# Performance work log

Hardware: AMD Instinct MI355X
Metric: run time of the kernel (lower is better)

The kernel has to match this reference:

```python
import jax, jax.numpy as jnp
import numpy as np

N = 100000
NEG_SLOPE = 0.2
EPS = 1e-16


def _gatconv(h_in, src, dst, W, a_src, a_dst, b):
    # h_in: [N, Fin]; src/dst: [E_tot] (self-loops included); W: [Fin, Fout]
    h = h_in @ W                                  # [N, Fout]
    alpha_s = h @ a_src                           # [N]
    alpha_d = h @ a_dst                           # [N]
    e = alpha_s[src] + alpha_d[dst]               # [E_tot]
    e = jnp.where(e > 0, e, NEG_SLOPE * e)        # leaky_relu
    m = jax.ops.segment_max(e, dst, num_segments=N)
    e = jnp.exp(e - m[dst])
    s = jax.ops.segment_sum(e, dst, num_segments=N)
    alpha = e / (s[dst] + EPS)                    # segment softmax over in-edges of each dst
    out = jax.ops.segment_sum(alpha[:, None] * h[src], dst, num_segments=N)
    return out + b


def setup_inputs() -> dict:
    key = jax.random.key(0)
    ks = jax.random.split(key, 10)
    Fin, Fh, Fo = 64, 64, 40
    E = 1600000
    x = jax.random.normal(ks[0], (N, Fin), dtype=jnp.float32)
    edge_index = jax.random.randint(ks[1], (2, E), 0, N, dtype=jnp.int64)
    g = 1.0 / np.sqrt(Fin)
    W1 = jax.random.uniform(ks[2], (Fin, Fh), jnp.float32, -g, g)
    a_src1 = jax.random.uniform(ks[3], (Fh,), jnp.float32, -g, g)
    a_dst1 = jax.random.uniform(ks[4], (Fh,), jnp.float32, -g, g)
    b1 = jnp.zeros((Fh,), jnp.float32)
    g2 = 1.0 / np.sqrt(Fh)
    W2 = jax.random.uniform(ks[5], (Fh, Fo), jnp.float32, -g2, g2)
    a_src2 = jax.random.uniform(ks[6], (Fo,), jnp.float32, -g2, g2)
    a_dst2 = jax.random.uniform(ks[7], (Fo,), jnp.float32, -g2, g2)
    b2 = jnp.zeros((Fo,), jnp.float32)
    return {"x": x, "edge_index": edge_index, "W1": W1, "a_src1": a_src1,
            "a_dst1": a_dst1, "b1": b1, "W2": W2, "a_src2": a_src2,
            "a_dst2": a_dst2, "b2": b2}


def reference(x, edge_index, W1, a_src1, a_dst1, b1, W2, a_src2, a_dst2, b2):
    # add self loops (PyG GATConv default)
    loops = jnp.arange(N, dtype=edge_index.dtype)
    src = jnp.concatenate([edge_index[0], loops])
    dst = jnp.concatenate([edge_index[1], loops])
    h = _gatconv(x, src, dst, W1, a_src1, a_dst1, b1)
    h = jax.nn.relu(h)  # dropout p=0 / eval -> no-op
    h = _gatconv(h, src, dst, W2, a_src2, a_dst2, b2)
    return jax.nn.log_softmax(h, axis=-1)
```

## Files before the change

### kernel.cpp

```cpp
#include <hip/hip_runtime.h>
#include <math.h>

#ifndef NEG_SLOPE
#define NEG_SLOPE 0.2f
#endif

#define BUCK_BITS 9
#define BUCK_SIZE 512
#define BUCK_CAP  12288
#define PA_ILP    8
#define SMAX      0x1FFFF

typedef __attribute__((ext_vector_type(8))) short bhalf8;
typedef __attribute__((ext_vector_type(4))) float f32x4;

__device__ __forceinline__ void get_edge(const void* ei, int is64, int e, int E,
                                         int& s, int& d) {
    if (e >= E) { s = e - E; d = s; return; }
    if (is64) {
        const long long* p = (const long long*)ei;
        s = (int)p[e];
        d = (int)p[(long long)E + e];
    } else {
        const int* p = (const int*)ei;
        s = p[e];
        d = p[E + e];
    }
}

__device__ __forceinline__ unsigned f2bf1(float x) {
    unsigned u = __float_as_uint(x);
    return (u + 0x7fffu + ((u >> 16) & 1u)) >> 16;
}

__global__ __launch_bounds__(256) void bin_gemm1(
    const void* __restrict__ ei, int E, int Etot, int binB, int gemmB, int period,
    int* __restrict__ fill, unsigned* __restrict__ pairs,
    const float* __restrict__ x, const float* __restrict__ W1,
    const float* __restrict__ avs, const float* __restrict__ avd,
    unsigned short* __restrict__ Hb, float* __restrict__ asn,
    float* __restrict__ adn, int N) {
    __shared__ __align__(16) char smem[4096];
    const int t = threadIdx.x;
    const int bi = blockIdx.x;
    const bool isBin = (bi % period) == 0;

    if (isBin) {
        const int bb = bi / period;
        int* cnt   = (int*)smem;
        int* goff  = cnt + 256;
        int* sflag = goff + 256;
        if (t < 64) {
            const int* p = (const int*)ei;
            int bad = 0;
            for (int j = 0; j < 4; ++j) bad |= (p[2 * (t * 4 + j) + 1] != 0);
            unsigned long long m = __ballot(bad);
            if (t == 0) *sflag = (m == 0ull) ? 1 : 0;
        }
        cnt[t] = 0;
        __syncthreads();
        const int is64 = *sflag;
        const int base = bb * (256 * PA_ILP) + t;
        int s[PA_ILP], d[PA_ILP], r[PA_ILP];
        bool ok[PA_ILP];
#pragma unroll
        for (int u = 0; u < PA_ILP; ++u) {
            int e = base + u * 256;
            ok[u] = (e < Etot);
            s[u] = d[u] = 0;
            if (ok[u]) get_edge(ei, is64, e, E, s[u], d[u]);
        }
#pragma unroll
        for (int u = 0; u < PA_ILP; ++u)
            if (ok[u]) r[u] = atomicAdd(&cnt[d[u] >> BUCK_BITS], 1);
        __syncthreads();
        if (cnt[t] > 0) goff[t] = atomicAdd(&fill[t], cnt[t]);
        __syncthreads();
#pragma unroll
        for (int u = 0; u < PA_ILP; ++u) {
            if (ok[u]) {
                int b = d[u] >> BUCK_BITS;
                int idx = goff[b] + r[u];
                if (idx < BUCK_CAP)
                    pairs[(size_t)b * BUCK_CAP + idx] =
                        (unsigned)s[u] | ((unsigned)(d[u] & (BUCK_SIZE - 1)) << 17);
            }
        }
    } else {
        const int gi = bi - bi / period - 1;
        if (gi >= gemmB) return;
        const int lane = t & 63;
        const int w    = t >> 6;
        const int rloc = lane & 15;
        const int kg   = lane >> 4;
        const int base = gi * 64;
        const int row  = base + w * 16 + rloc;
        const int rowc = (row < N) ? row : (N - 1);

        bhalf8 xh[2], xl[2];
        {
            const float* xr = x + (size_t)rowc * 64;
#pragma unroll
            for (int ks = 0; ks < 2; ++ks) {
                const int k0 = kg * 8 + ks * 32;
                float4 a0 = *(const float4*)(xr + k0);
                float4 a1 = *(const float4*)(xr + k0 + 4);
                float av[8] = {a0.x, a0.y, a0.z, a0.w, a1.x, a1.y, a1.z, a1.w};
                bhalf8 h8, l8;
#pragma unroll
                for (int j = 0; j < 8; ++j) {
                    unsigned hb_ = f2bf1(av[j]);
                    float hf = __uint_as_float(hb_ << 16);
                    h8[j] = (short)hb_;
                    l8[j] = (short)f2bf1(av[j] - hf);
                }
                xh[ks] = h8;
                xl[ks] = l8;
            }
        }

        f32x4 dacc[4];
#pragma unroll
        for (int ct = 0; ct < 4; ++ct) dacc[ct] = (f32x4){0.f, 0.f, 0.f, 0.f};

#pragma unroll
        for (int ct = 0; ct < 4; ++ct) {
            const int col = ct * 16 + rloc;
#pragma unroll
            for (int ks = 0; ks < 2; ++ks) {
                const int k0 = kg * 8 + ks * 32;
                bhalf8 bh, bl;
#pragma unroll
                for (int j = 0; j < 8; ++j) {
                    float wv_ = W1[(size_t)(k0 + j) * 64 + col];
                    unsigned hb_ = f2bf1(wv_);
                    float hf = __uint_as_float(hb_ << 16);
                    bh[j] = (short)hb_;
                    bl[j] = (short)f2bf1(wv_ - hf);
                }
                dacc[ct] = __builtin_amdgcn_mfma_f32_16x16x32_bf16(xh[ks], bh, dacc[ct], 0, 0, 0);
                dacc[ct] = __builtin_amdgcn_mfma_f32_16x16x32_bf16(xl[ks], bh, dacc[ct], 0, 0, 0);
                dacc[ct] = __builtin_amdgcn_mfma_f32_16x16x32_bf16(xh[ks], bl, dacc[ct], 0, 0, 0);
            }
        }

        float sa[4], sd[4];
#pragma unroll
        for (int ct = 0; ct < 4; ++ct) {
            sa[ct] = avs[ct * 16 + rloc];
            sd[ct] = avd[ct * 16 + rloc];
        }
#pragma unroll
        for (int i = 0; i < 4; ++i) {
            float ps = 0.f, pd = 0.f;
#pragma unroll
            for (int ct = 0; ct < 4; ++ct) {
                float h = dacc[ct][i];
                ps += h * sa[ct];
                pd += h * sd[ct];
            }
#pragma unroll
            for (int off = 1; off < 16; off <<= 1) {
                ps += __shfl_xor(ps, off);
                pd += __shfl_xor(pd, off);
            }
            const int gr = base + w * 16 + kg * 4 + i;
            if (gr < N) {
                if (rloc == 0) { asn[gr] = ps; adn[gr] = pd; }
#pragma unroll
                for (int ct = 0; ct < 4; ++ct)
                    Hb[(size_t)gr * 64 + ct * 16 + rloc] =
                        (unsigned short)f2bf1(dacc[ct][i]);
            }
        }
    }
}

__global__ __launch_bounds__(256) void bucket_csr(
    const unsigned* __restrict__ pairs, const int* __restrict__ fill,
    int* __restrict__ row_ptr, int* __restrict__ csr_src, int N, int nbuck) {
    __shared__ int cnt[BUCK_SIZE];
    __shared__ int offs[BUCK_SIZE];
    __shared__ int sbase[256];
    __shared__ int stot;
    const int t = threadIdx.x;
    if (t < 64) {
        int v[4];
        int loc = 0;
#pragma unroll
        for (int i = 0; i < 4; ++i) {
            int idx = t * 4 + i;
            v[i] = (idx < nbuck) ? fill[idx] : 0;
            loc += v[i];
        }
        int x = loc;
        for (int off = 1; off < 64; off <<= 1) {
            int y = __shfl_up(x, off);
            if (t >= off) x += y;
        }
        int run = x - loc;
#pragma unroll
        for (int i = 0; i < 4; ++i) {
            int idx = t * 4 + i;
            if (idx < 256) sbase[idx] = run;
            run += v[i];
        }
        if (t == 63) stot = x;
    }
    cnt[t] = 0; cnt[t + 256] = 0;
    __syncthreads();

    const int b = blockIdx.x;
    const int gb = sbase[b];
    int m = fill[b];
    if (m > BUCK_CAP) m = BUCK_CAP;
    if (b == 0 && t == 0) row_ptr[N] = stot;
    const unsigned* bp = pairs + (size_t)b * BUCK_CAP;

    int i = t;
    for (; i + 768 < m; i += 1024) {
        unsigned p0 = bp[i], p1 = bp[i + 256], p2 = bp[i + 512], p3 = bp[i + 768];
        atomicAdd(&cnt[p0 >> 17], 1);
        atomicAdd(&cnt[p1 >> 17], 1);
        atomicAdd(&cnt[p2 >> 17], 1);
        atomicAdd(&cnt[p3 >> 17], 1);
    }
    for (; i < m; i += 256) atomicAdd(&cnt[bp[i] >> 17], 1);
    __syncthreads();

    if (t < 64) {
        int v[8];
        int loc = 0;
#pragma unroll
        for (int j = 0; j < 8; ++j) { v[j] = cnt[t * 8 + j]; loc += v[j]; }
        int x = loc;
        for (int off = 1; off < 64; off <<= 1) {
            int y = __shfl_up(x, off);
            if (t >= off) x += y;
        }
        int run = x - loc;
#pragma unroll
        for (int j = 0; j < 8; ++j) { offs[t * 8 + j] = gb + run; run += v[j]; }
    }
    __syncthreads();

    const int base_d = b << BUCK_BITS;
    for (int k = t; k < BUCK_SIZE; k += 256) {
        int d = base_d + k;
        if (d < N) row_ptr[d] = offs[k];
    }
    __syncthreads();

    i = t;
    for (; i + 768 < m; i += 1024) {
        unsigned p0 = bp[i], p1 = bp[i + 256], p2 = bp[i + 512], p3 = bp[i + 768];
        csr_src[atomicAdd(&offs[p0 >> 17], 1)] = p0 & SMAX;
        csr_src[atomicAdd(&offs[p1 >> 17], 1)] = p1 & SMAX;
        csr_src[atomicAdd(&offs[p2 >> 17], 1)] = p2 & SMAX;
        csr_src[atomicAdd(&offs[p3 >> 17], 1)] = p3 & SMAX;
    }
    for (; i < m; i += 256) {
        unsigned p = bp[i];
        csr_src[atomicAdd(&offs[p >> 17], 1)] = p & SMAX;
    }
}

__device__ __forceinline__ void bf16x8_fma(uint4 hv, float w, float* acc) {
    const unsigned* u = (const unsigned*)&hv;
#pragma unroll
    for (int i = 0; i < 4; ++i) {
        float lo = __uint_as_float(u[i] << 16);
        float hi = __uint_as_float(u[i] & 0xffff0000u);
        acc[2 * i]     += w * lo;
        acc[2 * i + 1] += w * hi;
    }
}

__global__ __launch_bounds__(256) void agg1_gemm2(
    const int* __restrict__ row_ptr, const int* __restrict__ csr_src,
    const float* __restrict__ asn1, const float* __restrict__ adn1,
    const unsigned short* __restrict__ Hb, const float* __restrict__ b1,
    const float* __restrict__ W2, const float* __restrict__ a_s2,
    const float* __restrict__ a_d2, unsigned short* __restrict__ Hb2,
    float* __restrict__ asn2, float* __restrict__ adn2, int N) {
    __shared__ __align__(16) unsigned short rb16[16][72];
    __shared__ float sa2[48], sd2[48], sb1[64];
    __shared__ float sps3[3][16], spd3[3][16];
    const int t = threadIdx.x;
    if (t < 48) {
        sa2[t] = (t < 40) ? a_s2[t] : 0.f;
        sd2[t] = (t < 40) ? a_d2[t] : 0.f;
    }
    if (t >= 64 && t < 128) sb1[t - 64] = b1[t - 64];

    const int lane = t & 63;
    const int wv   = t >> 6;
    const int tile = (wv < 3) ? wv : 0;

    bhalf8 bfr[2];
    {
        const int col = tile * 16 + (lane & 15);
        const int kb  = (lane >> 4) * 8;
        const bool cv = col < 40;
#pragma unroll
        for (int ks = 0; ks < 2; ++ks) {
            bhalf8 bb;
#pragma unroll
            for (int j = 0; j < 8; ++j) {
                float v = cv ? W2[(size_t)(kb + 32 * ks + j) * 40 + col] : 0.f;
                bb[j] = (short)f2bf1(v);
            }
            bfr[ks] = bb;
        }
    }
    __syncthreads();

    const int sub     = lane & 15;
    const int half    = sub >> 3;
    const int q       = sub & 7;
    const int grpbase = lane & 48;
    const int slot    = t >> 4;
    const int node    = blockIdx.x * 16 + slot;
    const bool valid  = node < N;
    const int nd      = valid ? node : N - 1;

    const int r0 = row_ptr[nd], r1 = row_ptr[nd + 1];
    const int deg = r1 - r0;
    const float add = adn1[nd];

    float acc[8];
#pragma unroll
    for (int i = 0; i < 8; ++i) acc[i] = 0.f;

    int   sA = 0, sB = 0;
    float wA = 0.f, wB = 0.f;
    {
        const bool vA = sub < deg;
        const bool vB = 16 + sub < deg;
        if (vA) sA = csr_src[r0 + sub];
        if (vB) sB = csr_src[r0 + 16 + sub];
        float aA = vA ? asn1[sA] : 0.f;
        float aB = vB ? asn1[sB] : 0.f;
        if (vA) { float v = aA + add; v = v > 0.f ? v : NEG_SLOPE * v; wA = __expf(v); }
        if (vB) { float v = aB + add; v = v > 0.f ? v : NEG_SLOPE * v; wB = __expf(v); }
    }
    float Ssum = wA + wB;

    {
        const int cnt = deg < 16 ? deg : 16;
        int se[8]; float we[8]; uint4 hv[8];
#pragma unroll
        for (int k = 0; k < 8; ++k) {
            int e = 2 * k + half;
            int sl = grpbase | (e & 15);
            se[k] = __shfl(sA, sl);
            float wk = __shfl(wA, sl);
            we[k] = (e < cnt) ? wk : 0.f;
        }
#pragma unroll
        for (int k = 0; k < 4; ++k)
            hv[k] = *(const uint4*)(Hb + (((unsigned)se[k] << 6) | (unsigned)(q << 3)));
        if (cnt > 8) {
#pragma unroll
            for (int k = 4; k < 8; ++k)
                hv[k] = *(const uint4*)(Hb + (((unsigned)se[k] << 6) | (unsigned)(q << 3)));
        }
#pragma unroll
        for (int k = 0; k < 4; ++k) bf16x8_fma(hv[k], we[k], acc);
        if (cnt > 8) {
#pragma unroll
            for (int k = 4; k < 8; ++k) bf16x8_fma(hv[k], we[k], acc);
        }
    }
    if (deg > 16) {
        const int cnt = (deg - 16) < 16 ? (deg - 16) : 16;
// ... 39 lines not shown
            for (int k = 0; k < 4; ++k) {
                int e = j + 2 * k + half;
                int src_lane = grpbase | (e & 15);
                se[k] = __shfl(s, src_lane);
                float wk = __shfl(w, src_lane);
                we[k] = (e < cnt) ? wk : 0.f;
            }
#pragma unroll
            for (int k = 0; k < 4; ++k)
                hv[k] = *(const uint4*)(Hb + (((unsigned)se[k] << 6) | (unsigned)(q << 3)));
#pragma unroll
            for (int k = 0; k < 4; ++k) bf16x8_fma(hv[k], we[k], acc);
        }
    }
#pragma unroll
    for (int i = 0; i < 8; ++i) acc[i] += __shfl_xor(acc[i], 8);
#pragma unroll
    for (int off = 1; off < 16; off <<= 1) Ssum += __shfl_xor(Ssum, off);
    const float inv = 1.f / (Ssum + 1e-16f);

    if (half == 0) {
        unsigned pk[4];
#pragma unroll
        for (int i = 0; i < 4; ++i) {
            float v0 = fmaxf(acc[2 * i]     * inv + sb1[q * 8 + 2 * i],     0.f);
            float v1 = fmaxf(acc[2 * i + 1] * inv + sb1[q * 8 + 2 * i + 1], 0.f);
            pk[i] = f2bf1(v0) | (f2bf1(v1) << 16);
        }
        *(uint4*)&rb16[slot][q * 8] = make_uint4(pk[0], pk[1], pk[2], pk[3]);
    }
    __syncthreads();

    if (wv < 3) {
        f32x4 dacc = {0.f, 0.f, 0.f, 0.f};
#pragma unroll
        for (int ks = 0; ks < 2; ++ks) {
            bhalf8 afr = *(const bhalf8*)&rb16[lane & 15][(lane >> 4) * 8 + 32 * ks];
            dacc = __builtin_amdgcn_mfma_f32_16x16x32_bf16(afr, bfr[ks], dacc, 0, 0, 0);
        }
        const int f   = tile * 16 + (lane & 15);
        const float saf = sa2[f];
        const float sdf = sd2[f];
        float psl = 0.f, pdl = 0.f;
#pragma unroll
        for (int i = 0; i < 4; ++i) {
            psl = dacc[i] * saf;
            pdl = dacc[i] * sdf;
#pragma unroll
            for (int off = 1; off < 16; off <<= 1) {
                psl += __shfl_xor(psl, off);
                pdl += __shfl_xor(pdl, off);
            }
            const int m  = (lane >> 4) * 4 + i;
            if ((lane & 15) == 0) { sps3[tile][m] = psl; spd3[tile][m] = pdl; }
            const int nn = blockIdx.x * 16 + m;
            if (f < 40 && nn < N)
                Hb2[(size_t)nn * 40 + f] = (unsigned short)f2bf1(dacc[i]);
        }
    }
    __syncthreads();
    if (t < 16) {
        const int nn = blockIdx.x * 16 + t;
        if (nn < N) {
            asn2[nn] = sps3[0][t] + sps3[1][t] + sps3[2][t];
            adn2[nn] = spd3[0][t] + spd3[1][t] + spd3[2][t];
        }
    }
}

__global__ __launch_bounds__(256) void agg2_lsm(
    const int* __restrict__ row_ptr, const int* __restrict__ csr_src,
    const float* __restrict__ asn, const float* __restrict__ adn,
    const unsigned short* __restrict__ Hb, const float* __restrict__ bias,
    float* __restrict__ out, int N) {
    const int lane    = threadIdx.x & 63;
    const int sub     = lane & 15;
    const int esl     = sub / 5;
    const int q5      = sub - esl * 5;
    const bool act    = sub < 15;
    const int qc      = act ? q5 : 0;
    const float qmask = act ? 1.f : 0.f;
    const int grpbase = lane & 48;
    const int node    = blockIdx.x * 16 + (threadIdx.x >> 4);
    const bool valid  = node < N;
    const int nd      = valid ? node : N - 1;

    const int r0 = row_ptr[nd], r1 = row_ptr[nd + 1];
    const int deg = r1 - r0;
    const float add = adn[nd];

    float acc[8];
#pragma unroll
    for (int i = 0; i < 8; ++i) acc[i] = 0.f;

    int   sA = 0, sB = 0;
    float wA = 0.f, wB = 0.f;
    {
        const bool vA = sub < deg;
        const bool vB = 16 + sub < deg;
        if (vA) sA = csr_src[r0 + sub];
        if (vB) sB = csr_src[r0 + 16 + sub];
        float aA = vA ? asn[sA] : 0.f;
        float aB = vB ? asn[sB] : 0.f;
        if (vA) { float v = aA + add; v = v > 0.f ? v : NEG_SLOPE * v; wA = __expf(v); }
        if (vB) { float v = aB + add; v = v > 0.f ? v : NEG_SLOPE * v; wB = __expf(v); }
    }
    float Ssum = wA + wB;

    {
        const int cnt = deg < 16 ? deg : 16;
        int se[6]; float we[6]; uint4 hv[6];
#pragma unroll
        for (int kk = 0; kk < 6; ++kk) {
            int e  = 3 * kk + esl;
            int el = (e < 16) ? e : 15;
            se[kk] = __shfl(sA, grpbase | el);
            float wk = __shfl(wA, grpbase | el) * qmask;
            we[kk] = (e < cnt) ? wk : 0.f;
        }
#pragma unroll
        for (int kk = 0; kk < 4; ++kk)
            hv[kk] = *(const uint4*)(Hb + ((unsigned)se[kk] * 40u + (unsigned)(qc << 3)));
        if (cnt > 12) {
#pragma unroll
            for (int kk = 4; kk < 6; ++kk)
                hv[kk] = *(const uint4*)(Hb + ((unsigned)se[kk] * 40u + (unsigned)(qc << 3)));
        }
#pragma unroll
        for (int kk = 0; kk < 4; ++kk) bf16x8_fma(hv[kk], we[kk], acc);
        if (cnt > 12) {
#pragma unroll
            for (int kk = 4; kk < 6; ++kk) bf16x8_fma(hv[kk], we[kk], acc);
        }
    }
    if (deg > 16) {
        const int cnt = (deg - 16) < 16 ? (deg - 16) : 16;
// ... 34 lines not shown
        }
        Ssum += w;
        for (int j = 0; j < cnt; j += 12) {
            int se[4]; float we[4]; uint4 hv[4];
#pragma unroll
            for (int k = 0; k < 4; ++k) {
                int e  = j + 3 * k + esl;
                int el = (e < 16) ? e : 15;
                se[k] = __shfl(s, grpbase | el);
                float wk = __shfl(w, grpbase | el) * qmask;
                we[k] = (e < cnt) ? wk : 0.f;
            }
#pragma unroll
            for (int k = 0; k < 4; ++k)
                hv[k] = *(const uint4*)(Hb + ((unsigned)se[k] * 40u + (unsigned)(qc << 3)));
#pragma unroll
            for (int k = 0; k < 4; ++k) bf16x8_fma(hv[k], we[k], acc);
        }
    }
#pragma unroll
    for (int i = 0; i < 8; ++i) {
        float a1 = __shfl(acc[i], grpbase + q5 + 5);
        float a2 = __shfl(acc[i], grpbase + q5 + 10);
        acc[i] += a1 + a2;
    }
#pragma unroll
    for (int off = 1; off < 16; off <<= 1) Ssum += __shfl_xor(Ssum, off);
    const float inv = 1.f / (Ssum + 1e-16f);
    const bool owner = act && (esl == 0);

    float val[8];
#pragma unroll
    for (int i = 0; i < 8; ++i) val[i] = acc[i] * inv + bias[qc * 8 + i];
    float mx = -3.0e38f;
    if (owner) {
#pragma unroll
        for (int i = 0; i < 8; ++i) mx = fmaxf(mx, val[i]);
    }
#pragma unroll
    for (int off = 1; off <= 8; off <<= 1) mx = fmaxf(mx, __shfl_xor(mx, off));
    float sm = 0.f;
    if (owner) {
#pragma unroll
        for (int i = 0; i < 8; ++i) sm += __expf(val[i] - mx);
    }
#pragma unroll
    for (int off = 1; off <= 8; off <<= 1) sm += __shfl_xor(sm, off);
    float ls = logf(sm) + mx;
    if (valid && owner) {
        float* op = out + (size_t)node * 40 + q5 * 8;
        ((float4*)op)[0] = make_float4(val[0] - ls, val[1] - ls, val[2] - ls, val[3] - ls);
        ((float4*)op)[1] = make_float4(val[4] - ls, val[5] - ls, val[6] - ls, val[7] - ls);
    }
}

extern "C" void kernel_launch(void* const* d_in, const int* in_sizes, int n_in,
                              void* d_out, int out_size, void* d_ws, size_t ws_size,
                              hipStream_t stream) {
    const float* x   = (const float*)d_in[0];
    const void*  ei  = d_in[1];
    const float* W1  = (const float*)d_in[2];
    const float* as1 = (const float*)d_in[3];
    const float* ad1 = (const float*)d_in[4];
    const float* b1  = (const float*)d_in[5];
    const float* W2  = (const float*)d_in[6];
    const float* as2 = (const float*)d_in[7];
    const float* ad2 = (const float*)d_in[8];
    const float* b2  = (const float*)d_in[9];
    float* out = (float*)d_out;

    const int N     = in_sizes[0] / 64;
    const int E     = in_sizes[1] / 2;
    const int Etot  = E + N;
    const int nbuck = (N + BUCK_SIZE - 1) >> BUCK_BITS;

    float* ws = (float*)d_ws;
    unsigned short* hb  = (unsigned short*)ws;  ws += (size_t)N * 32;
    unsigned short* hb2 = (unsigned short*)ws;  ws += (size_t)N * 20;
    float* asn1 = ws;              ws += N;
    float* adn1 = ws;              ws += N;
    float* asn2 = ws;              ws += N;
    float* adn2 = ws;              ws += N;
    int* row_ptr = (int*)ws;       ws += N + 1;
    int* csr_src = (int*)ws;       ws += Etot;
    int* fill   = (int*)ws;        ws += 256;
    unsigned* pairs = (unsigned*)ws;  ws += (size_t)256 * BUCK_CAP;

    const int binB   = (Etot + 256 * PA_ILP - 1) / (256 * PA_ILP);
    const int gemmB  = (N + 63) / 64;
    const int period = gemmB / binB + 2;
    const int grid1  = binB * period;
    const int AGG_B  = (N + 15) / 16;

    hipMemsetAsync(fill, 0, 256 * sizeof(int), stream);
    bin_gemm1<<<grid1, 256, 0, stream>>>(
        ei, E, Etot, binB, gemmB, period, fill, pairs,
        x, W1, as1, ad1, hb, asn1, adn1, N);
    bucket_csr<<<nbuck, 256, 0, stream>>>(pairs, fill, row_ptr, csr_src, N, nbuck);
    agg1_gemm2<<<AGG_B, 256, 0, stream>>>(
        row_ptr, csr_src, asn1, adn1, hb, b1, W2, as2, ad2, hb2, asn2, adn2, N);
    agg2_lsm<<<AGG_B, 256, 0, stream>>>(
        row_ptr, csr_src, asn2, adn2, hb2, b2, out, N);
}
```

Baseline: 220.1 us.

## Fuse bucket-to-CSR pass with first GEMM instead of edge binning

Result: slower. 231.9 us (+5.4%).

```diff
diff --git a/kernel.cpp b/kernel.cpp
--- a/kernel.cpp
+++ b/kernel.cpp
@@ -33,58 +33,145 @@
     return (u + 0x7fffu + ((u >> 16) & 1u)) >> 16;
 }
 
-__global__ __launch_bounds__(256) void bin_gemm1(
-    const void* __restrict__ ei, int E, int Etot, int binB, int gemmB, int period,
-    int* __restrict__ fill, unsigned* __restrict__ pairs,
+__global__ __launch_bounds__(256) void bin_pass(
+    const void* __restrict__ ei, int E, int Etot,
+    int* __restrict__ fill, unsigned* __restrict__ pairs) {
+    __shared__ int cnt[256];
+    __shared__ int goff[256];
+    __shared__ int sflag;
+    const int t = threadIdx.x;
+    if (t < 64) {
+        const int* p = (const int*)ei;
+        int bad = 0;
+        for (int j = 0; j < 4; ++j) bad |= (p[2 * (t * 4 + j) + 1] != 0);
+        unsigned long long m = __ballot(bad);
+        if (t == 0) sflag = (m == 0ull) ? 1 : 0;
+    }
+    cnt[t] = 0;
+    __syncthreads();
+    const int is64 = sflag;
+    const int base = blockIdx.x * (256 * PA_ILP) + t;
+    int s[PA_ILP], d[PA_ILP], r[PA_ILP];
+    bool ok[PA_ILP];
+#pragma unroll
+    for (int u = 0; u < PA_ILP; ++u) {
+        int e = base + u * 256;
+        ok[u] = (e < Etot);
+        s[u] = d[u] = 0;
+        if (ok[u]) get_edge(ei, is64, e, E, s[u], d[u]);
+    }
+#pragma unroll
+    for (int u = 0; u < PA_ILP; ++u)
+        if (ok[u]) r[u] = atomicAdd(&cnt[d[u] >> BUCK_BITS], 1);
+    __syncthreads();
+    if (cnt[t] > 0) goff[t] = atomicAdd(&fill[t], cnt[t]);
+    __syncthreads();
+#pragma unroll
+    for (int u = 0; u < PA_ILP; ++u) {
+        if (ok[u]) {
+            int b = d[u] >> BUCK_BITS;
+            int idx = goff[b] + r[u];
+            if (idx < BUCK_CAP)
+                pairs[(size_t)b * BUCK_CAP + idx] =
+                    (unsigned)s[u] | ((unsigned)(d[u] & (BUCK_SIZE - 1)) << 17);
+        }
+    }
+}
+
+__global__ __launch_bounds__(256) void csr_gemm1(
+    const unsigned* __restrict__ pairs, const int* __restrict__ fill,
+    int* __restrict__ row_ptr, int* __restrict__ csr_src, int nbuck,
+    int gemmB, int period,
     const float* __restrict__ x, const float* __restrict__ W1,
     const float* __restrict__ avs, const float* __restrict__ avd,
     unsigned short* __restrict__ Hb, float* __restrict__ asn,
     float* __restrict__ adn, int N) {
-    __shared__ __align__(16) char smem[4096];
+    __shared__ int cnt[BUCK_SIZE];
+    __shared__ int offs[BUCK_SIZE];
+    __shared__ int sbase[256];
+    __shared__ int stot;
     const int t = threadIdx.x;
     const int bi = blockIdx.x;
-    const bool isBin = (bi % period) == 0;
-
-    if (isBin) {
-        const int bb = bi / period;
-        int* cnt   = (int*)smem;
-        int* goff  = cnt + 256;
-        int* sflag = goff + 256;
+
+    if ((bi % period) == 0) {
+        const int b = bi / period;
         if (t < 64) {
-            const int* p = (const int*)ei;
-            int bad = 0;
-            for (int j = 0; j < 4; ++j) bad |= (p[2 * (t * 4 + j) + 1] != 0);
-            unsigned long long m = __ballot(bad);
-            if (t == 0) *sflag = (m == 0ull) ? 1 : 0;
-        }
-        cnt[t] = 0;
+            int v[4];
+            int loc = 0;
+#pragma unroll
+            for (int i = 0; i < 4; ++i) {
+                int idx = t * 4 + i;
+                v[i] = (idx < nbuck) ? fill[idx] : 0;
+                loc += v[i];
+            }
+            int x_ = loc;
+            for (int off = 1; off < 64; off <<= 1) {
+                int y = __shfl_up(x_, off);
+                if (t >= off) x_ += y;
+            }
+            int run = x_ - loc;
+#pragma unroll
+            for (int i = 0; i < 4; ++i) {
+                int idx = t * 4 + i;
+                if (idx < 256) sbase[idx] = run;
+                run += v[i];
+            }
+            if (t == 63) stot = x_;
+        }
+        cnt[t] = 0; cnt[t + 256] = 0;
         __syncthreads();
-        const int is64 = *sflag;
-        const int base = bb * (256 * PA_ILP) + t;
-        int s[PA_ILP], d[PA_ILP], r[PA_ILP];
-        bool ok[PA_ILP];
-#pragma unroll
-        for (int u = 0; u < PA_ILP; ++u) {
-            int e = base + u * 256;
-            ok[u] = (e < Etot);
-            s[u] = d[u] = 0;
-            if (ok[u]) get_edge(ei, is64, e, E, s[u], d[u]);
-        }
-#pragma unroll
-        for (int u = 0; u < PA_ILP; ++u)
-            if (ok[u]) r[u] = atomicAdd(&cnt[d[u] >> BUCK_BITS], 1);
+
+        const int gb = sbase[b];
+        int m = fill[b];
+        if (m > BUCK_CAP) m = BUCK_CAP;
+        if (b == 0 && t == 0) row_ptr[N] = stot;
+        const unsigned* bp = pairs + (size_t)b * BUCK_CAP;
+
+        int i = t;
+        for (; i + 768 < m; i += 1024) {
+            unsigned p0 = bp[i], p1 = bp[i + 256], p2 = bp[i + 512], p3 = bp[i + 768];
+            atomicAdd(&cnt[p0 >> 17], 1);
+            atomicAdd(&cnt[p1 >> 17], 1);
+            atomicAdd(&cnt[p2 >> 17], 1);
+            atomicAdd(&cnt[p3 >> 17], 1);
+        }
+        for (; i < m; i += 256) atomicAdd(&cnt[bp[i] >> 17], 1);
         __syncthreads();
-        if (cnt[t] > 0) goff[t] = atomicAdd(&fill[t], cnt[t]);
+
+        if (t < 64) {
+            int v[8];
+            int loc = 0;
+#pragma unroll
+            for (int j = 0; j < 8; ++j) { v[j] = cnt[t * 8 + j]; loc += v[j]; }
+            int x_ = loc;
+            for (int off = 1; off < 64; off <<= 1) {
+                int y = __shfl_up(x_, off);
+                if (t >= off) x_ += y;
+            }
+            int run = x_ - loc;
+#pragma unroll
+            for (int j = 0; j < 8; ++j) { offs[t * 8 + j] = gb + run; run += v[j]; }
+        }
         __syncthreads();
-#pragma unroll
-        for (int u = 0; u < PA_ILP; ++u) {
-            if (ok[u]) {
-                int b = d[u] >> BUCK_BITS;
-                int idx = goff[b] + r[u];
-                if (idx < BUCK_CAP)
-                    pairs[(size_t)b * BUCK_CAP + idx] =
-                        (unsigned)s[u] | ((unsigned)(d[u] & (BUCK_SIZE - 1)) << 17);
-            }
+
+        const int base_d = b << BUCK_BITS;
+        for (int k = t; k < BUCK_SIZE; k += 256) {
+            int d = base_d + k;
+            if (d < N) row_ptr[d] = offs[k];
+        }
+        __syncthreads();
+
+        i = t;
+        for (; i + 768 < m; i += 1024) {
+            unsigned p0 = bp[i], p1 = bp[i + 256], p2 = bp[i + 512], p3 = bp[i + 768];
+            csr_src[atomicAdd(&offs[p0 >> 17], 1)] = p0 & SMAX;
+            csr_src[atomicAdd(&offs[p1 >> 17], 1)] = p1 & SMAX;
+            csr_src[atomicAdd(&offs[p2 >> 17], 1)] = p2 & SMAX;
+            csr_src[atomicAdd(&offs[p3 >> 17], 1)] = p3 & SMAX;
+        }
+        for (; i < m; i += 256) {
+            unsigned p = bp[i];
+            csr_src[atomicAdd(&offs[p >> 17], 1)] = p & SMAX;
         }
     } else {
         const int gi = bi - bi / period - 1;
@@ -173,95 +260,6 @@
                         (unsigned short)f2bf1(dacc[ct][i]);
             }
         }
-    }
-}
-
-__global__ __launch_bounds__(256) void bucket_csr(
-    const unsigned* __restrict__ pairs, const int* __restrict__ fill,
-    int* __restrict__ row_ptr, int* __restrict__ csr_src, int N, int nbuck) {
-    __shared__ int cnt[BUCK_SIZE];
-    __shared__ int offs[BUCK_SIZE];
-    __shared__ int sbase[256];
-    __shared__ int stot;
-    const int t = threadIdx.x;
-    if (t < 64) {
-        int v[4];
-        int loc = 0;
-#pragma unroll
-        for (int i = 0; i < 4; ++i) {
-            int idx = t * 4 + i;
-            v[i] = (idx < nbuck) ? fill[idx] : 0;
-            loc += v[i];
-        }
-        int x = loc;
-        for (int off = 1; off < 64; off <<= 1) {
-            int y = __shfl_up(x, off);
-            if (t >= off) x += y;
-        }
-        int run = x - loc;
-#pragma unroll
-        for (int i = 0; i < 4; ++i) {
-            int idx = t * 4 + i;
-            if (idx < 256) sbase[idx] = run;
-            run += v[i];
-        }
-        if (t == 63) stot = x;
-    }
-    cnt[t] = 0; cnt[t + 256] = 0;
-    __syncthreads();
-
-    const int b = blockIdx.x;
-    const int gb = sbase[b];
-    int m = fill[b];
-    if (m > BUCK_CAP) m = BUCK_CAP;
-    if (b == 0 && t == 0) row_ptr[N] = stot;
-    const unsigned* bp = pairs + (size_t)b * BUCK_CAP;
-
-    int i = t;
-    for (; i + 768 < m; i += 1024) {
-        unsigned p0 = bp[i], p1 = bp[i + 256], p2 = bp[i + 512], p3 = bp[i + 768];
-        atomicAdd(&cnt[p0 >> 17], 1);
-        atomicAdd(&cnt[p1 >> 17], 1);
-        atomicAdd(&cnt[p2 >> 17], 1);
-        atomicAdd(&cnt[p3 >> 17], 1);
-    }
-    for (; i < m; i += 256) atomicAdd(&cnt[bp[i] >> 17], 1);
-    __syncthreads();
-
-    if (t < 64) {
-        int v[8];
-        int loc = 0;
-#pragma unroll
-        for (int j = 0; j < 8; ++j) { v[j] = cnt[t * 8 + j]; loc += v[j]; }
-        int x = loc;
-        for (int off = 1; off < 64; off <<= 1) {
-            int y = __shfl_up(x, off);
-            if (t >= off) x += y;
-        }
-        int run = x - loc;
-#pragma unroll
-        for (int j = 0; j < 8; ++j) { offs[t * 8 + j] = gb + run; run += v[j]; }
-    }
-    __syncthreads();
-
-    const int base_d = b << BUCK_BITS;
-    for (int k = t; k < BUCK_SIZE; k += 256) {
-        int d = base_d + k;
-        if (d < N) row_ptr[d] = offs[k];
-    }
-    __syncthreads();
-
-    i = t;
-    for (; i + 768 < m; i += 1024) {
-        unsigned p0 = bp[i], p1 = bp[i + 256], p2 = bp[i + 512], p3 = bp[i + 768];
-        csr_src[atomicAdd(&offs[p0 >> 17], 1)] = p0 & SMAX;
-        csr_src[atomicAdd(&offs[p1 >> 17], 1)] = p1 & SMAX;
-        csr_src[atomicAdd(&offs[p2 >> 17], 1)] = p2 & SMAX;
-        csr_src[atomicAdd(&offs[p3 >> 17], 1)] = p3 & SMAX;
-    }
-    for (; i < m; i += 256) {
-        unsigned p = bp[i];
-        csr_src[atomicAdd(&offs[p >> 17], 1)] = p & SMAX;
     }
 }
 
@@ -670,17 +668,17 @@
     int* fill   = (int*)ws;        ws += 256;
     unsigned* pairs = (unsigned*)ws;  ws += (size_t)256 * BUCK_CAP;
 
-    const int binB   = (Etot + 256 * PA_ILP - 1) / (256 * PA_ILP);
-    const int gemmB  = (N + 63) / 64;
-    const int period = gemmB / binB + 2;
-    const int grid1  = binB * period;
-    const int AGG_B  = (N + 15) / 16;
+    const int binB    = (Etot + 256 * PA_ILP - 1) / (256 * PA_ILP);
+    const int gemmB   = (N + 63) / 64;
+    const int periodC = gemmB / nbuck + 2;
+    const int gridC   = nbuck * periodC;
+    const int AGG_B   = (N + 15) / 16;
 
     hipMemsetAsync(fill, 0, 256 * sizeof(int), stream);
-    bin_gemm1<<<grid1, 256, 0, stream>>>(
-        ei, E, Etot, binB, gemmB, period, fill, pairs,
+    bin_pass<<<binB, 256, 0, stream>>>(ei, E, Etot, fill, pairs);
+    csr_gemm1<<<gridC, 256, 0, stream>>>(
+        pairs, fill, row_ptr, csr_src, nbuck, gemmB, periodC,
         x, W1, as1, ad1, hb, asn1, adn1, N);
-    bucket_csr<<<nbuck, 256, 0, stream>>>(pairs, fill, row_ptr, csr_src, N, nbuck);
     agg1_gemm2<<<AGG_B, 256, 0, stream>>>(
         row_ptr, csr_src, asn1, adn1, hb, b1, W2, as2, ad2, hb2, asn2, adn2, N);
     agg2_lsm<<<AGG_B, 256, 0, stream>>>(
```

## Fuse all GAT stages into one persistent cooperative kernel with grid syncs

Applied to the files above, without the earlier changes.

Result: slower. 523.9 us (+138.0%).

```diff
diff --git a/kernel.cpp b/kernel.cpp
--- a/kernel.cpp
+++ b/kernel.cpp
@@ -1,5 +1,8 @@
 #include <hip/hip_runtime.h>
+#include <hip/hip_cooperative_groups.h>
 #include <math.h>
+
+namespace cg = cooperative_groups;
 
 #ifndef NEG_SLOPE
 #define NEG_SLOPE 0.2f
@@ -10,6 +13,7 @@
 #define BUCK_CAP  12288
 #define PA_ILP    8
 #define SMAX      0x1FFFF
+#define SMEM_BYTES 5248
 
 typedef __attribute__((ext_vector_type(8))) short bhalf8;
 typedef __attribute__((ext_vector_type(4))) float f32x4;
@@ -33,156 +37,158 @@
     return (u + 0x7fffu + ((u >> 16) & 1u)) >> 16;
 }
 
-__global__ __launch_bounds__(256) void bin_gemm1(
-    const void* __restrict__ ei, int E, int Etot, int binB, int gemmB, int period,
-    int* __restrict__ fill, unsigned* __restrict__ pairs,
-    const float* __restrict__ x, const float* __restrict__ W1,
-    const float* __restrict__ avs, const float* __restrict__ avd,
-    unsigned short* __restrict__ Hb, float* __restrict__ asn,
-    float* __restrict__ adn, int N) {
-    __shared__ __align__(16) char smem[4096];
+__device__ __forceinline__ void bf16x8_fma(uint4 hv, float w, float* acc) {
+    const unsigned* u = (const unsigned*)&hv;
+#pragma unroll
+    for (int i = 0; i < 4; ++i) {
+        float lo = __uint_as_float(u[i] << 16);
+        float hi = __uint_as_float(u[i] & 0xffff0000u);
+        acc[2 * i]     += w * lo;
+        acc[2 * i + 1] += w * hi;
+    }
+}
+
+
+__device__ __forceinline__ void bin_body(const void* ei, int E, int Etot, int bb,
+                                         int* fill, unsigned* pairs, char* smem) {
+    int* cnt   = (int*)smem;
+    int* goff  = cnt + 256;
+    int* sflag = goff + 256;
     const int t = threadIdx.x;
-    const int bi = blockIdx.x;
-    const bool isBin = (bi % period) == 0;
-
-    if (isBin) {
-        const int bb = bi / period;
-        int* cnt   = (int*)smem;
-        int* goff  = cnt + 256;
-        int* sflag = goff + 256;
-        if (t < 64) {
-            const int* p = (const int*)ei;
-            int bad = 0;
-            for (int j = 0; j < 4; ++j) bad |= (p[2 * (t * 4 + j) + 1] != 0);
-            unsigned long long m = __ballot(bad);
-            if (t == 0) *sflag = (m == 0ull) ? 1 : 0;
-        }
-        cnt[t] = 0;
-        __syncthreads();
-        const int is64 = *sflag;
-        const int base = bb * (256 * PA_ILP) + t;
-        int s[PA_ILP], d[PA_ILP], r[PA_ILP];
-        bool ok[PA_ILP];
-#pragma unroll
-        for (int u = 0; u < PA_ILP; ++u) {
-            int e = base + u * 256;
-            ok[u] = (e < Etot);
-            s[u] = d[u] = 0;
-            if (ok[u]) get_edge(ei, is64, e, E, s[u], d[u]);
-        }
-#pragma unroll
-        for (int u = 0; u < PA_ILP; ++u)
-            if (ok[u]) r[u] = atomicAdd(&cnt[d[u] >> BUCK_BITS], 1);
-        __syncthreads();
-        if (cnt[t] > 0) goff[t] = atomicAdd(&fill[t], cnt[t]);
-        __syncthreads();
-#pragma unroll
-        for (int u = 0; u < PA_ILP; ++u) {
-            if (ok[u]) {
-                int b = d[u] >> BUCK_BITS;
-                int idx = goff[b] + r[u];
-                if (idx < BUCK_CAP)
-                    pairs[(size_t)b * BUCK_CAP + idx] =
-                        (unsigned)s[u] | ((unsigned)(d[u] & (BUCK_SIZE - 1)) << 17);
+    if (t < 64) {
+        const int* p = (const int*)ei;
+        int bad = 0;
+        for (int j = 0; j < 4; ++j) bad |= (p[2 * (t * 4 + j) + 1] != 0);
+        unsigned long long m = __ballot(bad);
+        if (t == 0) *sflag = (m == 0ull) ? 1 : 0;
+    }
+    cnt[t] = 0;
+    __syncthreads();
+    const int is64 = *sflag;
+    const int base = bb * (256 * PA_ILP) + t;
+    int s[PA_ILP], d[PA_ILP], r[PA_ILP];
+    bool ok[PA_ILP];
+#pragma unroll
+    for (int u = 0; u < PA_ILP; ++u) {
+        int e = base + u * 256;
+        ok[u] = (e < Etot);
+        s[u] = d[u] = 0;
+        if (ok[u]) get_edge(ei, is64, e, E, s[u], d[u]);
+    }
+#pragma unroll
+    for (int u = 0; u < PA_ILP; ++u)
+        if (ok[u]) r[u] = atomicAdd(&cnt[d[u] >> BUCK_BITS], 1);
+    __syncthreads();
+    if (cnt[t] > 0) goff[t] = atomicAdd(&fill[t], cnt[t]);
+    __syncthreads();
+#pragma unroll
+    for (int u = 0; u < PA_ILP; ++u) {
+        if (ok[u]) {
+            int b = d[u] >> BUCK_BITS;
+            int idx = goff[b] + r[u];
+            if (idx < BUCK_CAP)
+                pairs[(size_t)b * BUCK_CAP + idx] =
+                    (unsigned)s[u] | ((unsigned)(d[u] & (BUCK_SIZE - 1)) << 17);
+        }
+    }
+}
+
+__device__ __forceinline__ void gemm_body(int gi, const float* x, const float* W1,
+        const float* avs, const float* avd, unsigned short* Hb,
+        float* asn, float* adn, int N) {
+    const int t    = threadIdx.x;
+    const int lane = t & 63;
+    const int w    = t >> 6;
+    const int rloc = lane & 15;
+    const int kg   = lane >> 4;
+    const int base = gi * 64;
+    const int row  = base + w * 16 + rloc;
+    const int rowc = (row < N) ? row : (N - 1);
+
+    bhalf8 xh[2], xl[2];
+    {
+        const float* xr = x + (size_t)rowc * 64;
+#pragma unroll
+        for (int ks = 0; ks < 2; ++ks) {
+            const int k0 = kg * 8 + ks * 32;
+            float4 a0 = *(const float4*)(xr + k0);
+            float4 a1 = *(const float4*)(xr + k0 + 4);
+            float av[8] = {a0.x, a0.y, a0.z, a0.w, a1.x, a1.y, a1.z, a1.w};
+            bhalf8 h8, l8;
+#pragma unroll
+            for (int j = 0; j < 8; ++j) {
+                unsigned hb_ = f2bf1(av[j]);
+                float hf = __uint_as_float(hb_ << 16);
+                h8[j] = (short)hb_;
+                l8[j] = (short)f2bf1(av[j] - hf);
             }
-        }
-    } else {
-        const int gi = bi - bi / period - 1;
-        if (gi >= gemmB) return;
-        const int lane = t & 63;
-        const int w    = t >> 6;
-        const int rloc = lane & 15;
-        const int kg   = lane >> 4;
-        const int base = gi * 64;
-        const int row  = base + w * 16 + rloc;
-        const int rowc = (row < N) ? row : (N - 1);
-
-        bhalf8 xh[2], xl[2];
-        {
-            const float* xr = x + (size_t)rowc * 64;
-#pragma unroll
-            for (int ks = 0; ks < 2; ++ks) {
-                const int k0 = kg * 8 + ks * 32;
-                float4 a0 = *(const float4*)(xr + k0);
-                float4 a1 = *(const float4*)(xr + k0 + 4);
-                float av[8] = {a0.x, a0.y, a0.z, a0.w, a1.x, a1.y, a1.z, a1.w};
-                bhalf8 h8, l8;
-#pragma unroll
-                for (int j = 0; j < 8; ++j) {
-                    unsigned hb_ = f2bf1(av[j]);
-                    float hf = __uint_as_float(hb_ << 16);
-                    h8[j] = (short)hb_;
-                    l8[j] = (short)f2bf1(av[j] - hf);
-                }
-                xh[ks] = h8;
-                xl[ks] = l8;
+            xh[ks] = h8;
+            xl[ks] = l8;
+        }
+    }
+
+    f32x4 dacc[4];
+#pragma unroll
+    for (int ct = 0; ct < 4; ++ct) dacc[ct] = (f32x4){0.f, 0.f, 0.f, 0.f};
+
+#pragma unroll
+    for (int ct = 0; ct < 4; ++ct) {
+        const int col = ct * 16 + rloc;
+#pragma unroll
+        for (int ks = 0; ks < 2; ++ks) {
+            const int k0 = kg * 8 + ks * 32;
+            bhalf8 bh, bl;
+#pragma unroll
+            for (int j = 0; j < 8; ++j) {
+                float wv_ = W1[(size_t)(k0 + j) * 64 + col];
+                unsigned hb_ = f2bf1(wv_);
+                float hf = __uint_as_float(hb_ << 16);
+                bh[j] = (short)hb_;
+                bl[j] = (short)f2bf1(wv_ - hf);
             }
-        }
-
-        f32x4 dacc[4];
-#pragma unroll
-        for (int ct = 0; ct < 4; ++ct) dacc[ct] = (f32x4){0.f, 0.f, 0.f, 0.f};
-
+            dacc[ct] = __builtin_amdgcn_mfma_f32_16x16x32_bf16(xh[ks], bh, dacc[ct], 0, 0, 0);
+            dacc[ct] = __builtin_amdgcn_mfma_f32_16x16x32_bf16(xl[ks], bh, dacc[ct], 0, 0, 0);
+            dacc[ct] = __builtin_amdgcn_mfma_f32_16x16x32_bf16(xh[ks], bl, dacc[ct], 0, 0, 0);
+        }
+    }
+
+    float sa[4], sd[4];
+#pragma unroll
+    for (int ct = 0; ct < 4; ++ct) {
+        sa[ct] = avs[ct * 16 + rloc];
+        sd[ct] = avd[ct * 16 + rloc];
+    }
+#pragma unroll
+    for (int i = 0; i < 4; ++i) {
+        float ps = 0.f, pd = 0.f;
 #pragma unroll
         for (int ct = 0; ct < 4; ++ct) {
-            const int col = ct * 16 + rloc;
-#pragma unroll
-            for (int ks = 0; ks < 2; ++ks) {
-                const int k0 = kg * 8 + ks * 32;
-                bhalf8 bh, bl;
-#pragma unroll
-                for (int j = 0; j < 8; ++j) {
-                    float wv_ = W1[(size_t)(k0 + j) * 64 + col];
-                    unsigned hb_ = f2bf1(wv_);
-                    float hf = __uint_as_float(hb_ << 16);
-                    bh[j] = (short)hb_;
-                    bl[j] = (short)f2bf1(wv_ - hf);
-                }
-                dacc[ct] = __builtin_amdgcn_mfma_f32_16x16x32_bf16(xh[ks], bh, dacc[ct], 0, 0, 0);
-                dacc[ct] = __builtin_amdgcn_mfma_f32_16x16x32_bf16(xl[ks], bh, dacc[ct], 0, 0, 0);
-                dacc[ct] = __builtin_amdgcn_mfma_f32_16x16x32_bf16(xh[ks], bl, dacc[ct], 0, 0, 0);
-            }
-        }
-
-        float sa[4], sd[4];
-#pragma unroll
-        for (int ct = 0; ct < 4; ++ct) {
-            sa[ct] = avs[ct * 16 + rloc];
-            sd[ct] = avd[ct * 16 + rloc];
-        }
-#pragma unroll
-        for (int i = 0; i < 4; ++i) {
-            float ps = 0.f, pd = 0.f;
-#pragma unroll
-            for (int ct = 0; ct < 4; ++ct) {
-                float h = dacc[ct][i];
-                ps += h * sa[ct];
-                pd += h * sd[ct];
-            }
-#pragma unroll
-            for (int off = 1; off < 16; off <<= 1) {
-                ps += __shfl_xor(ps, off);
-                pd += __shfl_xor(pd, off);
-            }
-            const int gr = base + w * 16 + kg * 4 + i;
-            if (gr < N) {
-                if (rloc == 0) { asn[gr] = ps; adn[gr] = pd; }
-#pragma unroll
-                for (int ct = 0; ct < 4; ++ct)
-                    Hb[(size_t)gr * 64 + ct * 16 + rloc] =
-                        (unsigned short)f2bf1(dacc[ct][i]);
-            }
-        }
-    }
-}
-
-__global__ __launch_bounds__(256) void bucket_csr(
-    const unsigned* __restrict__ pairs, const int* __restrict__ fill,
-    int* __restrict__ row_ptr, int* __restrict__ csr_src, int N, int nbuck) {
-    __shared__ int cnt[BUCK_SIZE];
-    __shared__ int offs[BUCK_SIZE];
-    __shared__ int sbase[256];
-    __shared__ int stot;
+            float h = dacc[ct][i];
+            ps += h * sa[ct];
+            pd += h * sd[ct];
+        }
+#pragma unroll
+        for (int off = 1; off < 16; off <<= 1) {
+            ps += __shfl_xor(ps, off);
+            pd += __shfl_xor(pd, off);
+        }
+        const int gr = base + w * 16 + kg * 4 + i;
+        if (gr < N) {
+            if (rloc == 0) { asn[gr] = ps; adn[gr] = pd; }
+#pragma unroll
+            for (int ct = 0; ct < 4; ++ct)
+                Hb[(size_t)gr * 64 + ct * 16 + rloc] =
+                    (unsigned short)f2bf1(dacc[ct][i]);
+        }
+    }
+}
+
+__device__ __forceinline__ void csr_body(const unsigned* pairs, const int* fill,
+        int* row_ptr, int* csr_src, int N, int nbuck, int b, char* smem) {
+    int* cnt   = (int*)smem;
+    int* offs  = cnt + 512;
+    int* sbase = offs + 512;
+    int* stot  = sbase + 256;
     const int t = threadIdx.x;
     if (t < 64) {
         int v[4];
@@ -205,16 +211,15 @@
             if (idx < 256) sbase[idx] = run;
             run += v[i];
         }
-        if (t == 63) stot = x;
+        if (t == 63) *stot = x;
     }
     cnt[t] = 0; cnt[t + 256] = 0;
     __syncthreads();
 
-    const int b = blockIdx.x;
     const int gb = sbase[b];
     int m = fill[b];
     if (m > BUCK_CAP) m = BUCK_CAP;
-    if (b == 0 && t == 0) row_ptr[N] = stot;
+    if (b == 0 && t == 0) row_ptr[N] = *stot;
     const unsigned* bp = pairs + (size_t)b * BUCK_CAP;
 
     int i = t;
@@ -265,62 +270,57 @@
     }
 }
 
-__device__ __forceinline__ void bf16x8_fma(uint4 hv, float w, float* acc) {
-    const unsigned* u = (const unsigned*)&hv;
-#pragma unroll
-    for (int i = 0; i < 4; ++i) {
-        float lo = __uint_as_float(u[i] << 16);
-        float hi = __uint_as_float(u[i] & 0xffff0000u);
-        acc[2 * i]     += w * lo;
-        acc[2 * i + 1] += w * hi;
-    }
-}
-
-__global__ __launch_bounds__(256) void agg1_gemm2(
-    const int* __restrict__ row_ptr, const int* __restrict__ csr_src,
-    const float* __restrict__ asn1, const float* __restrict__ adn1,
-    const unsigned short* __restrict__ Hb, const float* __restrict__ b1,
-    const float* __restrict__ W2, const float* __restrict__ a_s2,
-    const float* __restrict__ a_d2, unsigned short* __restrict__ Hb2,
-    float* __restrict__ asn2, float* __restrict__ adn2, int N) {
-    __shared__ __align__(16) unsigned short rb16[16][72];
-    __shared__ float sa2[48], sd2[48], sb1[64];
-    __shared__ float sps3[3][16], spd3[3][16];
+__device__ __forceinline__ void agg1_stage(const float* W2, const float* a_s2,
+        const float* a_d2, const float* b1, char* smem, bhalf8* bfr) {
     const int t = threadIdx.x;
+    float* sa2 = (float*)(smem + 2304);
+    float* sd2 = sa2 + 48;
+    float* sb1 = sd2 + 48;
     if (t < 48) {
         sa2[t] = (t < 40) ? a_s2[t] : 0.f;
         sd2[t] = (t < 40) ? a_d2[t] : 0.f;
     }
     if (t >= 64 && t < 128) sb1[t - 64] = b1[t - 64];
-
     const int lane = t & 63;
     const int wv   = t >> 6;
     const int tile = (wv < 3) ? wv : 0;
-
-    bhalf8 bfr[2];
-    {
-        const int col = tile * 16 + (lane & 15);
-        const int kb  = (lane >> 4) * 8;
-        const bool cv = col < 40;
-#pragma unroll
-        for (int ks = 0; ks < 2; ++ks) {
-            bhalf8 bb;
-#pragma unroll
-            for (int j = 0; j < 8; ++j) {
-                float v = cv ? W2[(size_t)(kb + 32 * ks + j) * 40 + col] : 0.f;
-                bb[j] = (short)f2bf1(v);
-            }
-            bfr[ks] = bb;
-        }
-    }
-    __syncthreads();
+    const int col  = tile * 16 + (lane & 15);
+    const int kb   = (lane >> 4) * 8;
+    const bool cv  = col < 40;
+#pragma unroll
+    for (int ks = 0; ks < 2; ++ks) {
+        bhalf8 bb;
+#pragma unroll
+        for (int j = 0; j < 8; ++j) {
+            float v = cv ? W2[(size_t)(kb + 32 * ks + j) * 40 + col] : 0.f;
+            bb[j] = (short)f2bf1(v);
+        }
+        bfr[ks] = bb;
+    }
+}
+
+__device__ __forceinline__ void agg1_body(int blk,
+        const int* row_ptr, const int* csr_src,
+        const float* asn1, const float* adn1, const unsigned short* Hb,
+        unsigned short* Hb2, float* asn2, float* adn2, int N,
+        char* smem, const bhalf8* bfr) {
+    unsigned short (*rb16)[72] = (unsigned short(*)[72])smem;
+    float* sa2  = (float*)(smem + 2304);
+    float* sd2  = sa2 + 48;
+    float* sb1  = sd2 + 48;
+    float* sps3 = sb1 + 64;
+    float* spd3 = sps3 + 48;
+    const int t    = threadIdx.x;
+    const int lane = t & 63;
+    const int wv   = t >> 6;
+    const int tile = (wv < 3) ? wv : 0;
 
     const int sub     = lane & 15;
     const int half    = sub >> 3;
     const int q       = sub & 7;
     const int grpbase = lane & 48;
     const int slot    = t >> 4;
-    const int node    = blockIdx.x * 16 + slot;
+    const int node    = blk * 16 + slot;
     const bool valid  = node < N;
     const int nd      = valid ? node : N - 1;
 
@@ -466,28 +466,28 @@
                 pdl += __shfl_xor(pdl, off);
             }
             const int m  = (lane >> 4) * 4 + i;
-            if ((lane & 15) == 0) { sps3[tile][m] = psl; spd3[tile][m] = pdl; }
-            const int nn = blockIdx.x * 16 + m;
+            if ((lane & 15) == 0) { sps3[tile * 16 + m] = psl; spd3[tile * 16 + m] = pdl; }
+            const int nn = blk * 16 + m;
             if (f < 40 && nn < N)
                 Hb2[(size_t)nn * 40 + f] = (unsigned short)f2bf1(dacc[i]);
         }
     }
     __syncthreads();
     if (t < 16) {
-        const int nn = blockIdx.x * 16 + t;
+        const int nn = blk * 16 + t;
         if (nn < N) {
-            asn2[nn] = sps3[0][t] + sps3[1][t] + sps3[2][t];
-            adn2[nn] = spd3[0][t] + spd3[1][t] + spd3[2][t];
-        }
-    }
-}
-
-__global__ __launch_bounds__(256) void agg2_lsm(
-    const int* __restrict__ row_ptr, const int* __restrict__ csr_src,
-    const float* __restrict__ asn, const float* __restrict__ adn,
-    const unsigned short* __restrict__ Hb, const float* __restrict__ bias,
-    float* __restrict__ out, int N) {
-    const int lane    = threadIdx.x & 63;
+            asn2[nn] = sps3[t] + sps3[16 + t] + sps3[32 + t];
+            adn2[nn] = spd3[t] + spd3[16 + t] + spd3[32 + t];
+        }
+    }
+}
+
+__device__ __forceinline__ void agg2_body(int blk,
+        const int* row_ptr, const int* csr_src,
+        const float* asn, const float* adn, const unsigned short* Hb,
+        const float* bias, float* out, int N) {
+    const int t       = threadIdx.x;
+    const int lane    = t & 63;
     const int sub     = lane & 15;
     const int esl     = sub / 5;
     const int q5      = sub - esl * 5;
@@ -495,7 +495,7 @@
     const int qc      = act ? q5 : 0;
     const float qmask = act ? 1.f : 0.f;
     const int grpbase = lane & 48;
-    const int node    = blockIdx.x * 16 + (threadIdx.x >> 4);
+    const int node    = blk * 16 + (t >> 4);
     const bool valid  = node < N;
     const int nd      = valid ? node : N - 1;
 
@@ -636,6 +636,115 @@
         ((float4*)op)[0] = make_float4(val[0] - ls, val[1] - ls, val[2] - ls, val[3] - ls);
         ((float4*)op)[1] = make_float4(val[4] - ls, val[5] - ls, val[6] - ls, val[7] - ls);
     }
+}
+
+struct FusedArgs {
+    const void* ei; int E; int Etot; int binB; int gemmB; int period; int grid1;
+    int* fill; unsigned* pairs;
+    const float* x; const float* W1; const float* as1; const float* ad1;
+    unsigned short* Hb; float* asn1; float* adn1;
+    int* row_ptr; int* csr_src; int nbuck;
+    const float* b1; const float* W2; const float* as2; const float* ad2;
+    unsigned short* Hb2; float* asn2; float* adn2;
+    const float* b2; float* out; int N; int aggB;
+};
+
+__global__ __launch_bounds__(256) void gat_fused(FusedArgs a) {
+    cg::grid_group grid = cg::this_grid();
+    __shared__ __align__(16) char smem[SMEM_BYTES];
+    const int t = threadIdx.x;
+
+    if (blockIdx.x == 0) a.fill[t] = 0;
+    grid.sync();
+
+    for (int vb = blockIdx.x; vb < a.grid1; vb += gridDim.x) {
+        if (vb % a.period == 0) {
+            bin_body(a.ei, a.E, a.Etot, vb / a.period, a.fill, a.pairs, smem);
+        } else {
+            int gi = vb - vb / a.period - 1;
+            if (gi < a.gemmB)
+                gemm_body(gi, a.x, a.W1, a.as1, a.ad1, a.Hb, a.asn1, a.adn1, a.N);
+        }
+        __syncthreads();
+    }
+    __threadfence();
+    grid.sync();
+
+    {
+        int spread = gridDim.x / a.nbuck;
+        if (spread < 1) spread = 1;
+        if ((int)(blockIdx.x) % spread == 0) {
+            int stride = gridDim.x / spread;
+            for (int v = blockIdx.x / spread; v < a.nbuck; v += stride) {
+                csr_body(a.pairs, a.fill, a.row_ptr, a.csr_src, a.N, a.nbuck, v, smem);
+                __syncthreads();
+            }
+        }
+    }
+    __threadfence();
+    grid.sync();
+
+    {
+        bhalf8 bfr[2];
+        agg1_stage(a.W2, a.as2, a.ad2, a.b1, smem, bfr);
+        __syncthreads();
+        for (int vb = blockIdx.x; vb < a.aggB; vb += gridDim.x) {
+            agg1_body(vb, a.row_ptr, a.csr_src, a.asn1, a.adn1, a.Hb,
+                      a.Hb2, a.asn2, a.adn2, a.N, smem, bfr);
+            __syncthreads();
+        }
+    }
+    __threadfence();
+    grid.sync();
+
+    for (int vb = blockIdx.x; vb < a.aggB; vb += gridDim.x)
+        agg2_body(vb, a.row_ptr, a.csr_src, a.asn2, a.adn2, a.Hb2, a.b2, a.out, a.N);
+}
+
+__global__ __launch_bounds__(256) void bin_gemm1_k(
+    const void* __restrict__ ei, int E, int Etot, int gemmB, int period,
+    int* __restrict__ fill, unsigned* __restrict__ pairs,
+    const float* __restrict__ x, const float* __restrict__ W1,
+    const float* __restrict__ avs, const float* __restrict__ avd,
+    unsigned short* __restrict__ Hb, float* __restrict__ asn,
+    float* __restrict__ adn, int N) {
+    __shared__ __align__(16) char smem[4096];
+    const int bi = blockIdx.x;
+    if ((bi % period) == 0) {
+        bin_body(ei, E, Etot, bi / period, fill, pairs, smem);
+    } else {
+        int gi = bi - bi / period - 1;
+        if (gi < gemmB) gemm_body(gi, x, W1, avs, avd, Hb, asn, adn, N);
+    }
+}
+
+__global__ __launch_bounds__(256) void bucket_csr_k(
+    const unsigned* __restrict__ pairs, const int* __restrict__ fill,
+    int* __restrict__ row_ptr, int* __restrict__ csr_src, int N, int nbuck) {
+    __shared__ __align__(16) char smem[SMEM_BYTES];
+    csr_body(pairs, fill, row_ptr, csr_src, N, nbuck, blockIdx.x, smem);
+}
+
+__global__ __launch_bounds__(256) void agg1_k(
+    const int* __restrict__ row_ptr, const int* __restrict__ csr_src,
+    const float* __restrict__ asn1, const float* __restrict__ adn1,
+    const unsigned short* __restrict__ Hb, const float* __restrict__ b1,
+    const float* __restrict__ W2, const float* __restrict__ a_s2,
+    const float* __restrict__ a_d2, unsigned short* __restrict__ Hb2,
+    float* __restrict__ asn2, float* __restrict__ adn2, int N) {
+    __shared__ __align__(16) char smem[3712];
+    bhalf8 bfr[2];
+    agg1_stage(W2, a_s2, a_d2, b1, smem, bfr);
+    __syncthreads();
+    agg1_body(blockIdx.x, row_ptr, csr_src, asn1, adn1, Hb, Hb2, asn2, adn2, N, smem, bfr);
+}
+
+__global__ __launch_bounds__(256) void agg2_k(
+    const int* __restrict__ row_ptr, const int* __restrict__ csr_src,
+    const float* __restrict__ asn, const float* __restrict__ adn,
+    const unsigned short* __restrict__ Hb, const float* __restrict__ bias,
+    float* __restrict__ out, int N) {
+    agg2_body(blockIdx.x, row_ptr, csr_src, asn, adn, Hb, bias, out, N);
 }
 
 extern "C" void kernel_launch(void* const* d_in, const int* in_sizes, int n_in,
@@ -674,15 +783,47 @@
     const int gemmB  = (N + 63) / 64;
     const int period = gemmB / binB + 2;
     const int grid1  = binB * period;
-    const int AGG_B  = (N + 15) / 16;
-
-    hipMemsetAsync(fill, 0, 256 * sizeof(int), stream);
-    bin_gemm1<<<grid1, 256, 0, stream>>>(
-        ei, E, Etot, binB, gemmB, period, fill, pairs,
-        x, W1, as1, ad1, hb, asn1, adn1, N);
-    bucket_csr<<<nbuck, 256, 0, stream>>>(pairs, fill, row_ptr, csr_src, N, nbuck);
-    agg1_gemm2<<<AGG_B, 256, 0, stream>>>(
-        row_ptr, csr_src, asn1, adn1, hb, b1, W2, as2, ad2, hb2, asn2, adn2, N);
-    agg2_lsm<<<AGG_B, 256, 0, stream>>>(
-        row_ptr, csr_src, asn2, adn2, hb2, b2, out, N);
-}
+    const int aggB   = (N + 15) / 16;
+
+    FusedArgs args;
+    args.ei = ei; args.E = E; args.Etot = Etot; args.binB = binB;
+    args.gemmB = gemmB; args.period = period; args.grid1 = grid1;
+    args.fill = fill; args.pairs = pairs;
+    args.x = x; args.W1 = W1; args.as1 = as1; args.ad1 = ad1;
+    args.Hb = hb; args.asn1 = asn1; args.adn1 = adn1;
+    args.row_ptr = row_ptr; args.csr_src = csr_src; args.nbuck = nbuck;
+    args.b1 = b1; args.W2 = W2; args.as2 = as2; args.ad2 = ad2;
+    args.Hb2 = hb2; args.asn2 = asn2; args.adn2 = adn2;
+    args.b2 = b2; args.out = out; args.N = N; args.aggB = aggB;
+
+    static int coopBlocksPerCU = -2;
+    if (coopBlocksPerCU == -2) {
+        int nb = 0;
+        hipError_t e = hipOccupancyMaxActiveBlocksPerMultiprocessor(
+            &nb, (const void*)gat_fused, 256, 0);
+        coopBlocksPerCU = (e == hipSuccess && nb >= 1) ? nb : 0;
+    }
+
+    bool launched = false;
+    if (coopBlocksPerCU > 0) {
+        int grid = coopBlocksPerCU * 256;
+        if (grid > aggB) grid = aggB;
+        void* kp[] = { (void*)&args };
+        hipError_t e = hipLaunchCooperativeKernel(
+            (const void*)gat_fused, dim3(grid), dim3(256), kp, 0, stream);
+        if (e == hipSuccess) launched = true;
+        else coopBlocksPerCU = 0;
+    }
+
+    if (!launched) {
+        hipMemsetAsync(fill, 0, 256 * sizeof(int), stream);
+        bin_gemm1_k<<<grid1, 256, 0, stream>>>(
+            ei, E, Etot, gemmB, period, fill, pairs,
+            x, W1, as1, ad1, hb, asn1, adn1, N);
+        bucket_csr_k<<<nbuck, 256, 0, stream>>>(pairs, fill, row_ptr, csr_src, N, nbuck);
+        agg1_k<<<aggB, 256, 0, stream>>>(
+            row_ptr, csr_src, asn1, adn1, hb, b1, W2, as2, ad2, hb2, asn2, adn2, N);
+        agg2_k<<<aggB, 256, 0, stream>>>(
+            row_ptr, csr_src, asn2, adn2, hb2, b2, out, N);
+    }
+}
```
